# Kernel optimization log

Measured on AMD Instinct MI355X. Metric: run time of the kernel, lower is better.

## Reference

```python
import jax, jax.numpy as jnp
import numpy as np

B, S, E, H = 4, 2048, 512, 8
D = E // H  # projection_dim per head


def setup_inputs() -> dict:
    key = jax.random.key(0)
    ks = jax.random.split(key, 5)
    scale = 1.0 / np.sqrt(E)
    return {
        "x": jax.random.normal(ks[0], (B, S, E), dtype=jnp.float32),
        "Wq": jax.random.normal(ks[1], (E, E), dtype=jnp.float32) * scale,
        "bq": jnp.zeros((E,), dtype=jnp.float32),
        "Wk": jax.random.normal(ks[2], (E, E), dtype=jnp.float32) * scale,
        "bk": jnp.zeros((E,), dtype=jnp.float32),
        "Wv": jax.random.normal(ks[3], (E, E), dtype=jnp.float32) * scale,
        "bv": jnp.zeros((E,), dtype=jnp.float32),
        "Wo": jax.random.normal(ks[4], (E, E), dtype=jnp.float32) * scale,
        "bo": jnp.zeros((E,), dtype=jnp.float32),
    }


def _split_heads(t):
    # [B,S,E] -> [B,H,S,D]
    b, s, _ = t.shape
    return t.reshape(b, s, H, D).transpose(0, 2, 1, 3)


def reference(x, Wq, bq, Wk, bk, Wv, bv, Wo, bo):
    q = _split_heads(x @ Wq + bq)  # [B,H,S,D]
    k = _split_heads(x @ Wk + bk)
    v = _split_heads(x @ Wv + bv)
    # materialized QK^T scores as in source: matmul -> scale -> softmax -> matmul
    score = jnp.einsum("bhqd,bhkd->bhqk", q, k) / jnp.sqrt(
        jnp.asarray(D, dtype=q.dtype)
    )
    weights = jax.nn.softmax(score, axis=-1)
    attn = jnp.einsum("bhqk,bhkd->bhqd", weights, v)  # [B,H,S,D]
    merged = attn.transpose(0, 2, 1, 3).reshape(x.shape[0], x.shape[1], E)
    return merged @ Wo + bo
```

## Files before the change

kernel.cpp:

```cpp
#include <hip/hip_runtime.h>
#include <hip/hip_bf16.h>
#include <stdint.h>

typedef __bf16 bf16;
typedef __bf16 bf16x2 __attribute__((ext_vector_type(2)));
typedef __bf16 bf16x4 __attribute__((ext_vector_type(4)));
typedef __bf16 bf16x8 __attribute__((ext_vector_type(8)));
typedef float f32x4 __attribute__((ext_vector_type(4)));
typedef float f32x16 __attribute__((ext_vector_type(16)));
typedef unsigned int u32x4 __attribute__((ext_vector_type(4)));

#define AS1 __attribute__((address_space(1)))
#define AS3 __attribute__((address_space(3)))


__global__ void cast_x_kernel(const float* __restrict__ x, bf16* __restrict__ xb) {
  int i = blockIdx.x * blockDim.x + threadIdx.x;
  float4 v = reinterpret_cast<const float4*>(x)[i];
  bf16x4 o = { (bf16)v.x, (bf16)v.y, (bf16)v.z, (bf16)v.w };
  *reinterpret_cast<bf16x4*>(xb + (size_t)i * 4) = o;
}

__global__ void transpose_w4_kernel(const float* __restrict__ W0, const float* __restrict__ W1,
                                    const float* __restrict__ W2, const float* __restrict__ W3,
                                    bf16* __restrict__ Wt) {
  __shared__ bf16 t[64][65];
  const float* W = blockIdx.z == 0 ? W0 : blockIdx.z == 1 ? W1 : blockIdx.z == 2 ? W2 : W3;
  bf16* dst = Wt + (size_t)blockIdx.z * 262144;
  const int c = threadIdx.x & 63, r0 = threadIdx.x >> 6;
  const int bn = blockIdx.x * 64, bk = blockIdx.y * 64;
#pragma unroll
  for (int i = 0; i < 16; ++i) {
    int r = r0 * 16 + i;
    t[c][r] = (bf16)W[(size_t)(bk + r) * 512 + bn + c];
  }
  __syncthreads();
#pragma unroll
  for (int i = 0; i < 16; ++i) {
    int n = r0 * 16 + i;
    dst[(size_t)(bn + n) * 512 + bk + c] = t[n][c];
  }
}

__device__ __forceinline__ void gemm_core(
    const bf16* __restrict__ A, const bf16* __restrict__ Bt, int m0, int n0,
    bf16* As, bf16* Bs, f32x4 (&acc)[4][4])
{
  const int tid = threadIdx.x;
  const int lane = tid & 63;
  const int w = tid >> 6;
  const int wm = w >> 1, wn = w & 1;
  const int cl = lane & 15, hi = lane >> 4;
  const int lr = lane >> 3;
  const int cofs = ((lane & 7) << 4) ^ (lr << 4);

  const char* Abase = (const char*)A;
  const char* Bbase = (const char*)Bt;

  for (int kt = 0; kt < 512; kt += 64) {
    __syncthreads();
#pragma unroll
    for (int c = 0; c < 4; ++c) {
      int rA = m0 + w * 32 + c * 8 + lr;
      const void* srcA = Abase + ((size_t)rA * 512 + kt) * 2 + cofs;
      void* dstA = (char*)As + w * 4096 + c * 1024;
      __builtin_amdgcn_global_load_lds((const AS1 void*)srcA, (AS3 void*)dstA, 16, 0, 0);
      int rB = n0 + w * 32 + c * 8 + lr;
      const void* srcB = Bbase + ((size_t)rB * 512 + kt) * 2 + cofs;
      void* dstB = (char*)Bs + w * 4096 + c * 1024;
      __builtin_amdgcn_global_load_lds((const AS1 void*)srcB, (AS3 void*)dstB, 16, 0, 0);
    }
    __syncthreads();
#pragma unroll
    for (int ks = 0; ks < 2; ++ks) {
      bf16x8 af[4], bfv[4];
#pragma unroll
      for (int mt = 0; mt < 4; ++mt) {
        int r = wm * 64 + mt * 16 + cl;
        int cb = (ks * 64 + (hi << 4)) ^ ((r & 7) << 4);
        af[mt] = *(const bf16x8*)((const char*)As + r * 128 + cb);
      }
#pragma unroll
      for (int nt = 0; nt < 4; ++nt) {
        int r = wn * 64 + nt * 16 + cl;
        int cb = (ks * 64 + (hi << 4)) ^ ((r & 7) << 4);
        bfv[nt] = *(const bf16x8*)((const char*)Bs + r * 128 + cb);
      }
#pragma unroll
      for (int mt = 0; mt < 4; ++mt)
#pragma unroll
        for (int nt = 0; nt < 4; ++nt)
          acc[mt][nt] = __builtin_amdgcn_mfma_f32_16x16x32_bf16(af[mt], bfv[nt], acc[mt][nt], 0, 0, 0);
    }
  }
}

__global__ __launch_bounds__(256) void gemm_qkv_kernel(
    const bf16* __restrict__ A, const bf16* __restrict__ Bt,
    const float* __restrict__ bq, const float* __restrict__ bk,
    const float* __restrict__ bv, bf16* __restrict__ qkv, float qscale)
{
  __shared__ bf16 As[128 * 64];
  __shared__ bf16 Bs[128 * 64];
  const int m0 = blockIdx.x * 128, n0 = blockIdx.y * 128;
  const int which = n0 >> 9;
  const float* bias = which == 0 ? bq : (which == 1 ? bk : bv);
  const float scale = which == 0 ? qscale : 1.0f;
  bf16* outb = qkv + (size_t)which * 4194304;
  const int ncol0 = n0 & 511;

  f32x4 acc[4][4] = {};
  gemm_core(A, Bt, m0, n0, As, Bs, acc);

  const int lane = threadIdx.x & 63, w = threadIdx.x >> 6;
  const int wm = w >> 1, wn = w & 1;
  const int cl = lane & 15, hi = lane >> 4;
#pragma unroll
  for (int mt = 0; mt < 4; ++mt) {
#pragma unroll
    for (int nt = 0; nt < 4; ++nt) {
      int row0 = m0 + wm * 64 + mt * 16 + hi * 4;
      int col = ncol0 + wn * 64 + nt * 16 + cl;
      float bvl = bias[col];
      int h = col >> 6, d = col & 63;
#pragma unroll
      for (int i = 0; i < 4; ++i) {
        float vv = (acc[mt][nt][i] + bvl) * scale;
        int row = row0 + i;
        int b = row >> 11, s = row & 2047;
        outb[(((size_t)(b * 8 + h)) * 2048 + s) * 64 + d] = (bf16)vv;
      }
    }
  }
}

__global__ __launch_bounds__(256) void gemm_out_kernel(
    const bf16* __restrict__ A, const bf16* __restrict__ Bt,
    const float* __restrict__ bias, float* __restrict__ out_f)
{
  __shared__ bf16 As[128 * 64];
  __shared__ bf16 Bs[128 * 64];
  const int m0 = blockIdx.x * 128, n0 = blockIdx.y * 128;

  f32x4 acc[4][4] = {};
  gemm_core(A, Bt, m0, n0, As, Bs, acc);

  const int lane = threadIdx.x & 63, w = threadIdx.x >> 6;
  const int wm = w >> 1, wn = w & 1;
  const int cl = lane & 15, hi = lane >> 4;
#pragma unroll
  for (int mt = 0; mt < 4; ++mt) {
#pragma unroll
    for (int nt = 0; nt < 4; ++nt) {
      int row0 = m0 + wm * 64 + mt * 16 + hi * 4;
      int col = n0 + wn * 64 + nt * 16 + cl;
      float bvl = bias[col];
#pragma unroll
      for (int i = 0; i < 4; ++i)
        out_f[(size_t)(row0 + i) * 512 + col] = acc[mt][nt][i] + bvl;
    }
  }
}

template<int NSPLIT>
__global__ __launch_bounds__(256, 4) void attn_kernel(
    const bf16* __restrict__ q, const bf16* __restrict__ k,
    const bf16* __restrict__ v, bf16* __restrict__ outp,
    float* __restrict__ Mpart, float* __restrict__ Lpart)
{
  __shared__ union SU {
    struct { bf16 K[2][4096]; bf16 V[2][4096]; } s;
    bf16 EP[4][2304];
  } u;
  __shared__ bf16 VT[4096];

  const int tid = threadIdx.x, lane = tid & 63, w = tid >> 6;
  const int l31 = lane & 31, H = lane >> 5;
  const int bh = blockIdx.x, qb = blockIdx.y, sp = blockIdx.z;
  const int b = bh >> 3, h = bh & 7;
  const int kvn = 2048 / NSPLIT;
  const int kv0 = sp * kvn;

  const bf16* Q  = q + (size_t)bh * 2048 * 64;
  const bf16* Kp = k + (size_t)bh * 2048 * 64;
  const bf16* Vp = v + (size_t)bh * 2048 * 64;

  const int q0 = qb * 128 + w * 32;
  const int kp = tid & 31;
  const int dblk = (tid >> 5) * 8;

  const int lr8 = lane >> 3;
  const int lc = lane & 7;

#define STAGE_KV(BUF, KEYBASE)                                                            \
  {                                                                                       \
    _Pragma("unroll")                                                                     \
    for (int i = 0; i < 2; ++i) {                                                         \
      int row = w * 16 + i * 8 + lr8;                                                     \
      const void* sK = (const char*)Kp + ((size_t)((KEYBASE) + row)) * 128 + ((lc ^ lr8) << 4); \
      void* dK = (char*)u.s.K[BUF] + w * 2048 + i * 1024;                                 \
      __builtin_amdgcn_global_load_lds((const AS1 void*)sK, (AS3 void*)dK, 16, 0, 0);     \
      const void* sV = (const char*)Vp + ((size_t)((KEYBASE) + row)) * 128 + ((lc ^ ((row >> 1) & 7)) << 4); \
      void* dV = (char*)u.s.V[BUF] + w * 2048 + i * 1024;                                 \
      __builtin_amdgcn_global_load_lds((const AS1 void*)sV, (AS3 void*)dV, 16, 0, 0);     \
    }                                                                                     \
  }

  bf16x8 qf[4];
#pragma unroll
  for (int s = 0; s < 4; ++s)
    qf[s] = *(const bf16x8*)(Q + (size_t)(q0 + l31) * 64 + s * 16 + H * 8);

  f32x16 oacc[2] = {};
  float m_run = -1e30f, l_run = 0.f;

  STAGE_KV(0, kv0);
  __syncthreads();

  int cur = 0;
  for (int kt0 = kv0; kt0 < kv0 + kvn; kt0 += 64) {
    {
      const char* vb = (const char*)u.s.V[cur];
      const int vofs = (((tid >> 5) ^ (kp & 7)) << 4);
      bf16x8 vs0 = *(const bf16x8*)(vb + (2 * kp) * 128 + vofs);
      bf16x8 vs1 = *(const bf16x8*)(vb + (2 * kp + 1) * 128 + vofs);
#pragma unroll
      for (int j = 0; j < 8; ++j) {
        int d = dblk + j;
        bf16x2 t = { vs0[j], vs1[j] };
        *(bf16x2*)((char*)VT + d * 128 + ((4 * kp) ^ ((d & 7) << 4))) = t;
      }
    }
    __syncthreads();

    if (kt0 + 64 < kv0 + kvn) STAGE_KV(cur ^ 1, kt0 + 64);

    const char* kb = (const char*)u.s.K[cur];

#pragma unroll
    for (int ct = 0; ct < 2; ++ct) {
      f32x16 sc = {};
      {
        const int krow = ct * 32 + l31;
        bf16x8 kf[4];
#pragma unroll
        for (int s = 0; s < 4; ++s)
          kf[s] = *(const bf16x8*)(kb + krow * 128 + ((s * 32 + H * 16) ^ ((l31 & 7) << 4)));
#pragma unroll
        for (int s = 0; s < 4; ++s)
          sc = __builtin_amdgcn_mfma_f32_32x32x16_bf16(kf[s], qf[s], sc, 0, 0, 0);
      }

      float mx[8];
#pragma unroll
      for (int r = 0; r < 8; ++r) mx[r] = fmaxf(sc[r], sc[r + 8]);
      float pmax = fmaxf(fmaxf(fmaxf(mx[0], mx[1]), fmaxf(mx[2], mx[3])),
                         fmaxf(fmaxf(mx[4], mx[5]), fmaxf(mx[6], mx[7])));
      pmax = fmaxf(pmax, __shfl_xor(pmax, 32));
      if (__any(pmax > m_run + 8.f)) {
        float mn = fmaxf(m_run, pmax);
        float alpha = exp2f(m_run - mn);
        m_run = mn;
        l_run *= alpha;
#pragma unroll
        for (int dt = 0; dt < 2; ++dt)
#pragma unroll
          for (int r = 0; r < 16; ++r) oacc[dt][r] *= alpha;
      }
#pragma unroll
      for (int r = 0; r < 16; ++r) sc[r] = exp2f(sc[r] - m_run);

      float sm[8];
#pragma unroll
      for (int r = 0; r < 8; ++r) sm[r] = sc[r] + sc[r + 8];
      float rs = ((sm[0] + sm[1]) + (sm[2] + sm[3])) + ((sm[4] + sm[5]) + (sm[6] + sm[7]));
      rs += __shfl_xor(rs, 32);
      l_run += rs;

#pragma unroll
      for (int half = 0; half < 2; ++half) {
        const int ks = ct * 2 + half;
        const int g0 = 8 * half;
        bf16x2 pa0 = { (bf16)sc[g0 + 0], (bf16)sc[g0 + 1] };
        bf16x2 pa1 = { (bf16)sc[g0 + 2], (bf16)sc[g0 + 3] };
        bf16x2 pb0 = { (bf16)sc[g0 + 4], (bf16)sc[g0 + 5] };
        bf16x2 pb1 = { (bf16)sc[g0 + 6], (bf16)sc[g0 + 7] };
        unsigned a0 = __builtin_bit_cast(unsigned, pa0);
        unsigned a1 = __builtin_bit_cast(unsigned, pa1);
        unsigned b0 = __builtin_bit_cast(unsigned, pb0);
        unsigned b1 = __builtin_bit_cast(unsigned, pb1);
        unsigned oa0 = (unsigned)__shfl_xor((int)a0, 32);
        unsigned oa1 = (unsigned)__shfl_xor((int)a1, 32);
        unsigned ob0 = (unsigned)__shfl_xor((int)b0, 32);
        unsigned ob1 = (unsigned)__shfl_xor((int)b1, 32);
        u32x4 pw = { H ? ob0 : a0, H ? ob1 : a1, H ? b0 : oa0, H ? b1 : oa1 };
        bf16x8 pf = __builtin_bit_cast(bf16x8, pw);
#pragma unroll
        for (int dt = 0; dt < 2; ++dt) {
          int d = dt * 32 + l31;
          bf16x8 vf = *(const bf16x8*)((const char*)VT + d * 128 + ((ks * 32 + H * 16) ^ ((d & 7) << 4)));
          oacc[dt] = __builtin_amdgcn_mfma_f32_32x32x16_bf16(vf, pf, oacc[dt], 0, 0, 0);
        }
      }
    }

    __syncthreads();
    cur ^= 1;
  }

  float inv_l = 1.0f / l_run;
#pragma unroll
  for (int dt = 0; dt < 2; ++dt)
#pragma unroll
    for (int r = 0; r < 16; ++r) {
      int d = dt * 32 + (r & 3) + 8 * (r >> 2) + 4 * H;
      u.EP[w][l31 * 72 + d] = (bf16)(oacc[dt][r] * inv_l);
    }
  __builtin_amdgcn_s_waitcnt(0);
  if (NSPLIT == 1) {
#pragma unroll
    for (int g = 0; g < 4; ++g) {
      int qr = g * 8 + (lane >> 3);
      bf16x8 row = *(const bf16x8*)&u.EP[w][qr * 72 + (lane & 7) * 8];
      *(bf16x8*)(outp + (size_t)(b * 2048 + q0 + qr) * 512 + h * 64 + (lane & 7) * 8) = row;
    }
  } else {
    bf16* op = outp + (size_t)sp * 65536 * 64;
#pragma unroll
    for (int g = 0; g < 4; ++g) {
      int qr = g * 8 + (lane >> 3);
      bf16x8 row = *(const bf16x8*)&u.EP[w][qr * 72 + (lane & 7) * 8];
      *(bf16x8*)(op + ((size_t)bh * 2048 + q0 + qr) * 64 + (lane & 7) * 8) = row;
    }
    if (H == 0) {
      size_t idx = (size_t)sp * 65536 + (size_t)bh * 2048 + q0 + l31;
      Mpart[idx] = m_run;
      Lpart[idx] = l_run;
    }
  }
#undef STAGE_KV
}

__global__ void merge_kernel(const bf16* __restrict__ Op, const float* __restrict__ Mp,
                             const float* __restrict__ Lp, bf16* __restrict__ merged) {
  int t = blockIdx.x * blockDim.x + threadIdx.x;
  int g = t & 7;
  int qq = (t >> 3) & 2047;
  int bh = t >> 14;
  int b = bh >> 3, h = bh & 7;
  size_t row = (size_t)bh * 2048 + qq;
  float m0 = Mp[row], m1 = Mp[65536 + row];
  float l0 = Lp[row], l1 = Lp[65536 + row];
  float M = fmaxf(m0, m1);
  float w0 = exp2f(m0 - M) * l0, w1 = exp2f(m1 - M) * l1;
  float inv = 1.f / (w0 + w1);
  w0 *= inv; w1 *= inv;
  bf16x8 a = *(const bf16x8*)(Op + row * 64 + g * 8);
  bf16x8 c = *(const bf16x8*)(Op + (size_t)65536 * 64 + row * 64 + g * 8);
  bf16x8 o;
#pragma unroll
  for (int j = 0; j < 8; ++j) o[j] = (bf16)(w0 * (float)a[j] + w1 * (float)c[j]);
  *(bf16x8*)(merged + ((size_t)(b * 2048 + qq)) * 512 + h * 64 + g * 8) = o;
}

extern "C" void kernel_launch(void* const* d_in, const int* in_sizes, int n_in,
                              void* d_out, int out_size, void* d_ws, size_t ws_size,
                              hipStream_t stream) {
  const float* x  = (const float*)d_in[0];
  const float* Wq = (const float*)d_in[1];
  const float* bq = (const float*)d_in[2];
  const float* Wk = (const float*)d_in[3];
  const float* bk = (const float*)d_in[4];
  const float* Wv = (const float*)d_in[5];
  const float* bv = (const float*)d_in[6];
  const float* Wo = (const float*)d_in[7];
  const float* bo = (const float*)d_in[8];
  float* out = (float*)d_out;

  char* ws = (char*)d_ws;
  bf16* xb  = (bf16*)(ws);
  bf16* wt  = (bf16*)(ws + 8388608);
  bf16* qkv = (bf16*)(ws + 10485760);
  bf16* mg  = (bf16*)(ws + 35651584);
  bf16* op  = (bf16*)(ws + 44040192);
  float* Mp = (float*)(ws + 60817408);
  float* Lp = (float*)(ws + 61341696);

  cast_x_kernel<<<4096, 256, 0, stream>>>(x, xb);
  transpose_w4_kernel<<<dim3(8, 8, 4), 256, 0, stream>>>(Wq, Wk, Wv, Wo, wt);

  const float qscale = 0.125f * 1.44269504088896f;
  gemm_qkv_kernel<<<dim3(64, 12), 256, 0, stream>>>(xb, wt, bq, bk, bv, qkv, qscale);

  bf16* qs = qkv;
  bf16* kk = qkv + 4194304;
  bf16* vv = qkv + 8388608;

  if (ws_size >= 61865984ull) {
    attn_kernel<2><<<dim3(32, 16, 2), 256, 0, stream>>>(qs, kk, vv, op, Mp, Lp);
    merge_kernel<<<2048, 256, 0, stream>>>(op, Mp, Lp, mg);
  } else {
    attn_kernel<1><<<dim3(32, 16, 1), 256, 0, stream>>>(qs, kk, vv, mg, nullptr, nullptr);
  }

  gemm_out_kernel<<<dim3(64, 4), 256, 0, stream>>>(mg, wt + 786432, bo, out);
}
```

Before: 120.0 us.

## Merge split-KV attention halves inside one 512-thread block via LDS

Replaces the two-way split-KV attention launch plus separate merge kernel with a single 512-thread block in which two groups of four waves each process half of the keys for the same query tile. The partial max, sum and output accumulators are combined through shared memory before a single bf16 write. This removes the global round trip of partial outputs and the extra merge launch. In exchange it doubles shared memory per block and puts block-wide barriers on both halves, which may lower occupancy.

```diff
diff --git a/kernel.cpp b/kernel.cpp
--- a/kernel.cpp
+++ b/kernel.cpp
@@ -162,32 +162,36 @@
   }
 }
 
-template<int NSPLIT>
-__global__ __launch_bounds__(256, 4) void attn_kernel(
+__global__ __launch_bounds__(512, 4) void attn_kernel(
     const bf16* __restrict__ q, const bf16* __restrict__ k,
-    const bf16* __restrict__ v, bf16* __restrict__ outp,
-    float* __restrict__ Mpart, float* __restrict__ Lpart)
+    const bf16* __restrict__ v, bf16* __restrict__ merged)
 {
   __shared__ union SU {
-    struct { bf16 K[2][4096]; bf16 V[2][4096]; } s;
-    bf16 EP[4][2304];
+    struct { bf16 K[2][2][4096]; bf16 V[2][2][4096]; } s;
+    struct {
+      float EPf[4][64][33];
+      float Msh[8][32];
+      float Lsh[8][32];
+      bf16  EP[4][2304];
+    } e;
   } u;
-  __shared__ bf16 VT[4096];
+  __shared__ bf16 VT[2][4096];
 
   const int tid = threadIdx.x, lane = tid & 63, w = tid >> 6;
+  const int wl = w & 3, half = w >> 2;
+  const int ht = tid & 255;
   const int l31 = lane & 31, H = lane >> 5;
-  const int bh = blockIdx.x, qb = blockIdx.y, sp = blockIdx.z;
+  const int bh = blockIdx.x, qb = blockIdx.y;
   const int b = bh >> 3, h = bh & 7;
-  const int kvn = 2048 / NSPLIT;
-  const int kv0 = sp * kvn;
+  const int kv0 = half << 10;
 
   const bf16* Q  = q + (size_t)bh * 2048 * 64;
   const bf16* Kp = k + (size_t)bh * 2048 * 64;
   const bf16* Vp = v + (size_t)bh * 2048 * 64;
 
-  const int q0 = qb * 128 + w * 32;
-  const int kp = tid & 31;
-  const int dblk = (tid >> 5) * 8;
+  const int q0 = qb * 128 + wl * 32;
+  const int kp = ht & 31;
+  const int dblk = (ht >> 5) * 8;
 
   const int lr8 = lane >> 3;
   const int lc = lane & 7;
@@ -196,12 +200,12 @@
   {                                                                                       \
     _Pragma("unroll")                                                                     \
     for (int i = 0; i < 2; ++i) {                                                         \
-      int row = w * 16 + i * 8 + lr8;                                                     \
+      int row = wl * 16 + i * 8 + lr8;                                                    \
       const void* sK = (const char*)Kp + ((size_t)((KEYBASE) + row)) * 128 + ((lc ^ lr8) << 4); \
-      void* dK = (char*)u.s.K[BUF] + w * 2048 + i * 1024;                                 \
+      void* dK = (char*)u.s.K[half][BUF] + wl * 2048 + i * 1024;                          \
       __builtin_amdgcn_global_load_lds((const AS1 void*)sK, (AS3 void*)dK, 16, 0, 0);     \
       const void* sV = (const char*)Vp + ((size_t)((KEYBASE) + row)) * 128 + ((lc ^ ((row >> 1) & 7)) << 4); \
-      void* dV = (char*)u.s.V[BUF] + w * 2048 + i * 1024;                                 \
+      void* dV = (char*)u.s.V[half][BUF] + wl * 2048 + i * 1024;                          \
       __builtin_amdgcn_global_load_lds((const AS1 void*)sV, (AS3 void*)dV, 16, 0, 0);     \
     }                                                                                     \
   }
@@ -218,24 +222,24 @@
   __syncthreads();
 
   int cur = 0;
-  for (int kt0 = kv0; kt0 < kv0 + kvn; kt0 += 64) {
+  for (int kt0 = kv0; kt0 < kv0 + 1024; kt0 += 64) {
     {
-      const char* vb = (const char*)u.s.V[cur];
-      const int vofs = (((tid >> 5) ^ (kp & 7)) << 4);
+      const char* vb = (const char*)u.s.V[half][cur];
+      const int vofs = (((ht >> 5) ^ (kp & 7)) << 4);
       bf16x8 vs0 = *(const bf16x8*)(vb + (2 * kp) * 128 + vofs);
       bf16x8 vs1 = *(const bf16x8*)(vb + (2 * kp + 1) * 128 + vofs);
 #pragma unroll
       for (int j = 0; j < 8; ++j) {
         int d = dblk + j;
         bf16x2 t = { vs0[j], vs1[j] };
-        *(bf16x2*)((char*)VT + d * 128 + ((4 * kp) ^ ((d & 7) << 4))) = t;
+        *(bf16x2*)((char*)&VT[half][0] + d * 128 + ((4 * kp) ^ ((d & 7) << 4))) = t;
       }
     }
     __syncthreads();
 
-    if (kt0 + 64 < kv0 + kvn) STAGE_KV(cur ^ 1, kt0 + 64);
-
-    const char* kb = (const char*)u.s.K[cur];
+    if (kt0 + 64 < kv0 + 1024) STAGE_KV(cur ^ 1, kt0 + 64);
+
+    const char* kb = (const char*)u.s.K[half][cur];
 
 #pragma unroll
     for (int ct = 0; ct < 2; ++ct) {
@@ -278,9 +282,9 @@
       l_run += rs;
 
 #pragma unroll
-      for (int half = 0; half < 2; ++half) {
-        const int ks = ct * 2 + half;
-        const int g0 = 8 * half;
+      for (int hf = 0; hf < 2; ++hf) {
+        const int ks = ct * 2 + hf;
+        const int g0 = 8 * hf;
         bf16x2 pa0 = { (bf16)sc[g0 + 0], (bf16)sc[g0 + 1] };
         bf16x2 pa1 = { (bf16)sc[g0 + 2], (bf16)sc[g0 + 3] };
         bf16x2 pb0 = { (bf16)sc[g0 + 4], (bf16)sc[g0 + 5] };
@@ -298,7 +302,7 @@
 #pragma unroll
         for (int dt = 0; dt < 2; ++dt) {
           int d = dt * 32 + l31;
-          bf16x8 vf = *(const bf16x8*)((const char*)VT + d * 128 + ((ks * 32 + H * 16) ^ ((d & 7) << 4)));
+          bf16x8 vf = *(const bf16x8*)((const char*)&VT[half][0] + d * 128 + ((ks * 32 + H * 16) ^ ((d & 7) << 4)));
           oacc[dt] = __builtin_amdgcn_mfma_f32_32x32x16_bf16(vf, pf, oacc[dt], 0, 0, 0);
         }
       }
@@ -308,59 +312,40 @@
     cur ^= 1;
   }
 
-  float inv_l = 1.0f / l_run;
-#pragma unroll
-  for (int dt = 0; dt < 2; ++dt)
-#pragma unroll
-    for (int r = 0; r < 16; ++r) {
-      int d = dt * 32 + (r & 3) + 8 * (r >> 2) + 4 * H;
-      u.EP[w][l31 * 72 + d] = (bf16)(oacc[dt][r] * inv_l);
-    }
-  __builtin_amdgcn_s_waitcnt(0);
-  if (NSPLIT == 1) {
+  if (H == 0) { u.e.Msh[w][l31] = m_run; u.e.Lsh[w][l31] = l_run; }
+  __syncthreads();
+  const int pw = w ^ 4;
+  float m_o = u.e.Msh[pw][l31], l_o = u.e.Lsh[pw][l31];
+  float Mt = fmaxf(m_run, m_o);
+  float denom = exp2f(m_run - Mt) * l_run + exp2f(m_o - Mt) * l_o;
+  float scale = exp2f(m_run - Mt) / denom;
+  if (w < 4) {
+    float* ep = &u.e.EPf[wl][lane][0];
+#pragma unroll
+    for (int dt = 0; dt < 2; ++dt)
+#pragma unroll
+      for (int r = 0; r < 16; ++r) ep[dt * 16 + r] = oacc[dt][r] * scale;
+  }
+  __syncthreads();
+  if (w >= 4) {
+    const float* ep = &u.e.EPf[wl][lane][0];
+#pragma unroll
+    for (int dt = 0; dt < 2; ++dt)
+#pragma unroll
+      for (int r = 0; r < 16; ++r) {
+        float val = ep[dt * 16 + r] + oacc[dt][r] * scale;
+        int d = dt * 32 + (r & 3) + 8 * (r >> 2) + 4 * H;
+        u.e.EP[wl][l31 * 72 + d] = (bf16)val;
+      }
+    __builtin_amdgcn_s_waitcnt(0);
 #pragma unroll
     for (int g = 0; g < 4; ++g) {
       int qr = g * 8 + (lane >> 3);
-      bf16x8 row = *(const bf16x8*)&u.EP[w][qr * 72 + (lane & 7) * 8];
-      *(bf16x8*)(outp + (size_t)(b * 2048 + q0 + qr) * 512 + h * 64 + (lane & 7) * 8) = row;
-    }
-  } else {
-    bf16* op = outp + (size_t)sp * 65536 * 64;
-#pragma unroll
-    for (int g = 0; g < 4; ++g) {
-      int qr = g * 8 + (lane >> 3);
-      bf16x8 row = *(const bf16x8*)&u.EP[w][qr * 72 + (lane & 7) * 8];
-      *(bf16x8*)(op + ((size_t)bh * 2048 + q0 + qr) * 64 + (lane & 7) * 8) = row;
-    }
-    if (H == 0) {
-      size_t idx = (size_t)sp * 65536 + (size_t)bh * 2048 + q0 + l31;
-      Mpart[idx] = m_run;
-      Lpart[idx] = l_run;
+      bf16x8 row = *(const bf16x8*)&u.e.EP[wl][qr * 72 + (lane & 7) * 8];
+      *(bf16x8*)(merged + (size_t)(b * 2048 + q0 + qr) * 512 + h * 64 + (lane & 7) * 8) = row;
     }
   }
 #undef STAGE_KV
-}
-
-__global__ void merge_kernel(const bf16* __restrict__ Op, const float* __restrict__ Mp,
-                             const float* __restrict__ Lp, bf16* __restrict__ merged) {
-  int t = blockIdx.x * blockDim.x + threadIdx.x;
-  int g = t & 7;
-  int qq = (t >> 3) & 2047;
-  int bh = t >> 14;
-  int b = bh >> 3, h = bh & 7;
-  size_t row = (size_t)bh * 2048 + qq;
-  float m0 = Mp[row], m1 = Mp[65536 + row];
-  float l0 = Lp[row], l1 = Lp[65536 + row];
-  float M = fmaxf(m0, m1);
-  float w0 = exp2f(m0 - M) * l0, w1 = exp2f(m1 - M) * l1;
-  float inv = 1.f / (w0 + w1);
-  w0 *= inv; w1 *= inv;
-  bf16x8 a = *(const bf16x8*)(Op + row * 64 + g * 8);
-  bf16x8 c = *(const bf16x8*)(Op + (size_t)65536 * 64 + row * 64 + g * 8);
-  bf16x8 o;
-#pragma unroll
-  for (int j = 0; j < 8; ++j) o[j] = (bf16)(w0 * (float)a[j] + w1 * (float)c[j]);
-  *(bf16x8*)(merged + ((size_t)(b * 2048 + qq)) * 512 + h * 64 + g * 8) = o;
 }
 
 extern "C" void kernel_launch(void* const* d_in, const int* in_sizes, int n_in,
@@ -382,9 +367,6 @@
   bf16* wt  = (bf16*)(ws + 8388608);
   bf16* qkv = (bf16*)(ws + 10485760);
   bf16* mg  = (bf16*)(ws + 35651584);
-  bf16* op  = (bf16*)(ws + 44040192);
-  float* Mp = (float*)(ws + 60817408);
-  float* Lp = (float*)(ws + 61341696);
 
   cast_x_kernel<<<4096, 256, 0, stream>>>(x, xb);
   transpose_w4_kernel<<<dim3(8, 8, 4), 256, 0, stream>>>(Wq, Wk, Wv, Wo, wt);
@@ -396,12 +378,7 @@
   bf16* kk = qkv + 4194304;
   bf16* vv = qkv + 8388608;
 
-  if (ws_size >= 61865984ull) {
-    attn_kernel<2><<<dim3(32, 16, 2), 256, 0, stream>>>(qs, kk, vv, op, Mp, Lp);
-    merge_kernel<<<2048, 256, 0, stream>>>(op, Mp, Lp, mg);
-  } else {
-    attn_kernel<1><<<dim3(32, 16, 1), 256, 0, stream>>>(qs, kk, vv, mg, nullptr, nullptr);
-  }
+  attn_kernel<<<dim3(32, 16), 512, 0, stream>>>(qs, kk, vv, mg);
 
   gemm_out_kernel<<<dim3(64, 4), 256, 0, stream>>>(mg, wt + 786432, bo, out);
 }
```

Measured after the change: 116.9 us. -2.6%, faster.
